# Optimization experiments

Measured on AMD Instinct MI355X. Metric: run time of the kernel, lower is better.

## Reference

```python
import jax, jax.numpy as jnp
import numpy as np

NUM_HEAD = 8
HIDDEN = 128
INPUT_DIM = 256
N1 = 1024
N2 = 1024
BATCH = 16


def setup_inputs() -> dict:
    key = jax.random.key(0)
    ks = jax.random.split(key, 10)
    HD = HIDDEN * NUM_HEAD  # 1024
    return {
        "x1": jax.random.normal(ks[0], (BATCH, N1, INPUT_DIM), jnp.float32),
        "x2": jax.random.normal(ks[1], (BATCH, N2, INPUT_DIM), jnp.float32),
        "B": jax.random.normal(ks[2], (N1, N2), jnp.float32),
        "wq_w": jax.random.normal(ks[3], (HD, INPUT_DIM), jnp.float32) * 0.02,
        "wq_b": jnp.zeros((HD,), jnp.float32),
        "wk_w": jax.random.normal(ks[4], (HD, INPUT_DIM), jnp.float32) * 0.02,
        "wk_b": jnp.zeros((HD,), jnp.float32),
        "wv_w": jax.random.normal(ks[5], (HD, INPUT_DIM), jnp.float32) * 0.02,
        "wv_b": jnp.zeros((HD,), jnp.float32),
        "proj_w": jax.random.normal(ks[6], (HIDDEN, HD), jnp.float32) * 0.02,
        "proj_b": jnp.zeros((HIDDEN,), jnp.float32),
    }


def reference(x1, x2, B, wq_w, wq_b, wk_w, wk_b, wv_w, wv_b, proj_w, proj_b):
    b, n1, _ = x1.shape
    n2 = x2.shape[1]
    sdk = jnp.sqrt(jnp.asarray(HIDDEN, x1.dtype))
    # Linear layers (torch convention: y = x @ W.T + b)
    q = x1 @ wq_w.T + wq_b                      # [b, n1, H*D]
    k = x2 @ wk_w.T + wk_b                      # [b, n2, H*D]
    v = x2 @ wv_w.T + wv_b                      # [b, n2, H*D]
    q = q.reshape(b, n1, NUM_HEAD, HIDDEN)
    k = k.reshape(b, n2, NUM_HEAD, HIDDEN)
    v = v.reshape(b, n2, NUM_HEAD, HIDDEN)
    # scores: [b, h, n1, n2]
    scores = jnp.einsum("bnhd,bmhd->bhnm", q, k) / sdk + B[None, None, :, :]
    attn = jax.nn.softmax(scores, axis=-1)
    out = jnp.einsum("bhnm,bmhd->bnhd", attn, v).reshape(b, n1, NUM_HEAD * HIDDEN)
    return out @ proj_w.T + proj_b              # [b, n1, HIDDEN]
```

## Files before the change

kernel.cpp:

```cpp
#include <hip/hip_runtime.h>
#include <hip/hip_fp16.h>

typedef _Float16 f16;
typedef __attribute__((ext_vector_type(4))) _Float16 f16x4;
typedef __attribute__((ext_vector_type(8))) _Float16 f16x8;
typedef __attribute__((ext_vector_type(4))) float f32x4;

#define MFMA_F16(a,b,c) __builtin_amdgcn_mfma_f32_16x16x32_f16((a),(b),(c),0,0,0)

__device__ __forceinline__ void gl_lds16(const f16* g, f16* l) {
  __builtin_amdgcn_global_load_lds(
      (const __attribute__((address_space(1))) unsigned int*)g,
      (__attribute__((address_space(3))) unsigned int*)l, 16, 0, 0);
}


__global__ __launch_bounds__(256) void conv_pack(
    const float* __restrict__ x1, const float* __restrict__ x2,
    const float* __restrict__ wq, const float* __restrict__ wk,
    const float* __restrict__ wv,
    f16* __restrict__ x1p, f16* __restrict__ x2p, f16* __restrict__ wp) {
  __shared__ f16 S[128][264];
  const int id = blockIdx.x, tid = threadIdx.x;
  const float* src;
  f16* dst;
  if (id < 128) {
    src = x1 + (size_t)id * 32768; dst = x1p + (size_t)id * 32768;
  } else if (id < 256) {
    src = x2 + (size_t)(id - 128) * 32768; dst = x2p + (size_t)(id - 128) * 32768;
  } else {
    const int wsel = (id - 256) >> 3, wt = (id - 256) & 7;
    const float* wsrc = (wsel == 0) ? wq : (wsel == 1) ? wk : wv;
    src = wsrc + (size_t)wt * 32768;
    dst = wp + (size_t)wsel * 262144 + (size_t)wt * 32768;
  }
#pragma unroll 8
  for (int i = 0; i < 32; i++) {
    int f = i * 256 + tid;
    int row = f >> 6, c4 = f & 63;
    float4 v = *(const float4*)(src + (size_t)row * 256 + c4 * 4);
    f16x4 hh; hh[0] = (f16)v.x; hh[1] = (f16)v.y; hh[2] = (f16)v.z; hh[3] = (f16)v.w;
    *(f16x4*)&S[row][c4 * 4] = hh;
  }
  __syncthreads();
#pragma unroll 8
  for (int i = 0; i < 16; i++) {
    int u = i * 256 + tid;
    int chunk = u >> 6, l2 = u & 63;
    int q = l2 >> 4, c = l2 & 15;
    int row = (chunk >> 3) * 16 + c, k = (chunk & 7) * 32 + q * 8;
    f16x8 v = *(const f16x8*)&S[row][k];
    *(f16x8*)(dst + (size_t)u * 8) = v;
  }
}

__global__ __launch_bounds__(512) __attribute__((amdgpu_waves_per_eu(4, 4)))
void gemm_qkv(const f16* __restrict__ x1p, const f16* __restrict__ x2p,
              const f16* __restrict__ wp,
              const float* __restrict__ wqb, const float* __restrict__ wkb,
              const float* __restrict__ wvb,
              f16* __restrict__ Qp, f16* __restrict__ Kp, f16* __restrict__ Vp,
              float qscale) {
  __shared__ f16 Wl[2][8192];
  __shared__ f16 Xl[2][8192];
  const int z = blockIdx.z;
  const f16* Xp = (z == 0) ? x1p : x2p;
  const float* bias = (z == 0) ? wqb : (z == 1) ? wkb : wvb;
  f16* outp = (z == 0) ? Qp : (z == 1) ? Kp : Vp;
  const float sc = (z == 0) ? qscale : 1.0f;

  const int tid = threadIdx.x, lane = tid & 63, wid = tid >> 6;
  const int col = lane & 15, quad = lane >> 4;
  const int xt = blockIdx.x, h = blockIdx.y;
  const int wr = wid >> 2, xc = wid & 3;
  const f16* Xb = Xp + (size_t)xt * 32768;
  const f16* Wb = wp + (size_t)z * 262144 + (size_t)h * 32768;

#define QISSUE(T, bufi)                                                   \
  {                                                                       \
    _Pragma("unroll") for (int j = 0; j < 2; j++) {                       \
      int lc = wid * 2 + j;                                               \
      int rt = lc >> 1, ksl = lc & 1;                                     \
      gl_lds16(Wb + (size_t)((rt * 8 + (T) * 2 + ksl) << 9) + lane * 8,   \
               &Wl[bufi][lc * 512]);                                      \
      gl_lds16(Xb + (size_t)((rt * 8 + (T) * 2 + ksl) << 9) + lane * 8,   \
               &Xl[bufi][lc * 512]);                                      \
    }                                                                     \
  }

  QISSUE(0, 0);
  QISSUE(1, 1);

  f32x4 acc[4][2];
#pragma unroll
  for (int i = 0; i < 4; i++)
#pragma unroll
    for (int j = 0; j < 2; j++) acc[i][j] = (f32x4){0.f, 0.f, 0.f, 0.f};

  __syncthreads();

  for (int t = 0; t < 4; ++t) {
    const int buf = t & 1;
    const f16* Ra = (z == 2) ? Xl[buf] : Wl[buf];
    const f16* Cb = (z == 2) ? Wl[buf] : Xl[buf];
#pragma unroll
    for (int ksl = 0; ksl < 2; ksl++) {
      f16x8 af[4], bf[2];
#pragma unroll
      for (int i = 0; i < 4; i++)
        af[i] = *(const f16x8*)&Ra[((wr * 4 + i) * 2 + ksl) * 512 + lane * 8];
#pragma unroll
      for (int j = 0; j < 2; j++)
        bf[j] = *(const f16x8*)&Cb[((xc * 2 + j) * 2 + ksl) * 512 + lane * 8];
#pragma unroll
      for (int i = 0; i < 4; i++)
#pragma unroll
        for (int j = 0; j < 2; j++) acc[i][j] = MFMA_F16(af[i], bf[j], acc[i][j]);
    }
    __syncthreads();
    if (t + 2 < 4) QISSUE(t + 2, buf);
  }

  if (z < 2) {
#pragma unroll
    for (int i = 0; i < 4; i++) {
      const int k0h = wr * 64 + i * 16 + quad * 4;
      float4 bq = *(const float4*)(bias + h * 128 + k0h);
      const int ks2 = k0h >> 5, q2 = (k0h >> 3) & 3, lo = k0h & 7;
#pragma unroll
      for (int j = 0; j < 2; j++) {
        const int bn2 = xt * 128 + xc * 32 + j * 16 + col;
        const int b = bn2 >> 10, n2 = bn2 & 1023;
        const int T = n2 >> 6, jt = (n2 >> 4) & 3, c2 = n2 & 15;
        f16x4 pk;
#pragma unroll
        for (int r = 0; r < 4; r++)
          pk[r] = (f16)((acc[i][j][r] + ((const float*)&bq)[r]) * sc);
        *(f16x4*)(outp + (size_t)(b * 8 + h) * 131072 + T * 8192 +
                  (jt * 4 + ks2) * 512 + (q2 * 16 + c2) * 8 + lo) = pk;
      }
    }
  } else {
#pragma unroll
    for (int j = 0; j < 2; j++) {
      const int d = xc * 32 + j * 16 + col;
      const float bv = bias[h * 128 + d];
      const int ct = d >> 4, cc = d & 15;
#pragma unroll
      for (int i = 0; i < 4; i++) {
        const int bn2 = xt * 128 + wr * 64 + i * 16 + quad * 4;
        const int b = bn2 >> 10, n2 = bn2 & 1023;
        const int T = n2 >> 6, kv6 = n2 & 63;
        const int ks2 = kv6 >> 5, qv = (kv6 >> 3) & 3, jj = kv6 & 7;
        f16x4 pk;
#pragma unroll
        for (int r = 0; r < 4; r++) pk[r] = (f16)(acc[i][j][r] + bv);
        *(f16x4*)(outp + (size_t)(b * 8 + h) * 131072 + T * 8192 +
                  (ct * 2 + ks2) * 512 + (qv * 16 + cc) * 8 + jj) = pk;
      }
    }
  }
}

__global__ __launch_bounds__(256) void gemm_proj(const f16* __restrict__ A,
                                                 const float* __restrict__ W,
                                                 const float* __restrict__ bias,
                                                 float* __restrict__ out) {
  constexpr int LD = 72;
  __shared__ f16 As[64][LD];
  __shared__ f16 Bs[64][LD];
  const int tid = threadIdx.x, lane = tid & 63, wid = tid >> 6;
  const int col = lane & 15, quad = lane >> 4;
  const int wm = (wid >> 1) * 32, wn = (wid & 1) * 32;
  const int m0 = blockIdx.x * 64, n0 = blockIdx.y * 64;

  f32x4 acc[2][2];
#pragma unroll
  for (int i = 0; i < 2; i++)
#pragma unroll
    for (int j = 0; j < 2; j++) acc[i][j] = (f32x4){0.f, 0.f, 0.f, 0.f};

  for (int kt = 0; kt < 16; ++kt) {
    const int k0 = kt * 64;
#pragma unroll
    for (int i = 0; i < 2; i++) {
      int f = i * 256 + tid;
      int r = f >> 3, ch = f & 7;
      *(f16x8*)&As[r][ch * 8] = *(const f16x8*)(A + (size_t)(m0 + r) * 1024 + k0 + ch * 8);
    }
#pragma unroll
    for (int i = 0; i < 4; i++) {
      int f = i * 256 + tid;
      int r = f >> 4, c4 = f & 15;
      float4 v = *(const float4*)(W + (size_t)(n0 + r) * 1024 + k0 + c4 * 4);
      f16x4 hh; hh[0] = (f16)v.x; hh[1] = (f16)v.y; hh[2] = (f16)v.z; hh[3] = (f16)v.w;
      *(f16x4*)&Bs[r][c4 * 4] = hh;
    }
    __syncthreads();
#pragma unroll
    for (int ks = 0; ks < 2; ks++) {
      f16x8 af[2], bf[2];
#pragma unroll
      for (int i = 0; i < 2; i++) af[i] = *(const f16x8*)&As[wm + i * 16 + col][ks * 32 + quad * 8];
#pragma unroll
      for (int j = 0; j < 2; j++) bf[j] = *(const f16x8*)&Bs[wn + j * 16 + col][ks * 32 + quad * 8];
#pragma unroll
      for (int i = 0; i < 2; i++)
#pragma unroll
        for (int j = 0; j < 2; j++) acc[i][j] = MFMA_F16(af[i], bf[j], acc[i][j]);
    }
    __syncthreads();
  }
#pragma unroll
  for (int j = 0; j < 2; j++) {
    const int c = n0 + wn + j * 16 + col;
    const float bv = bias[c];
#pragma unroll
    for (int i = 0; i < 2; i++) {
      const int r0 = m0 + wm + i * 16 + quad * 4;
#pragma unroll
      for (int r = 0; r < 4; r++)
        out[(size_t)(r0 + r) * 128 + c] = acc[i][j][r] + bv;
    }
  }
}

__global__ __launch_bounds__(512) __attribute__((amdgpu_waves_per_eu(4, 4)))
void attn_fused(const f16* __restrict__ Qp, const f16* __restrict__ Kp,
                const f16* __restrict__ Vp, const float* __restrict__ Bm,
                f16* __restrict__ O) {
  __shared__ f16 Ksl[2][8192];
  __shared__ f16 Vtl[2][8192];
  __shared__ f16 Ps[8192];
  const int tid = threadIdx.x, lane = tid & 63, wid = tid >> 6;
  const int col = lane & 15, quad = lane >> 4;
  const int id = blockIdx.x;
  const int mt = (id >> 3) & 7;
  const int bh = ((id >> 6) << 3) | (id & 7);
  const int b = bh >> 3, h = bh & 7;
  const int m0 = mt * 128;
  const int wm = wid * 16;

  const f16* Qb = Qp + (size_t)bh * 131072;
  const f16* Kb = Kp + (size_t)bh * 131072;
  const f16* Vb = Vp + (size_t)bh * 131072;

#define AISSUE(T, bufi)                                                       \
  {                                                                           \
    if (wid < 4) {                                                            \
      _Pragma("unroll") for (int j = 0; j < 4; j++)                           \
          gl_lds16(Kb + (size_t)(T) * 8192 + (wid * 4 + j) * 512 + lane * 8,  \
                   &Ksl[bufi][(wid * 4 + j) * 512]);                          \
    } else {                                                                  \
      _Pragma("unroll") for (int j = 0; j < 4; j++)                           \
          gl_lds16(Vb + (size_t)(T) * 8192 + ((wid - 4) * 4 + j) * 512 + lane * 8, \
                   &Vtl[bufi][((wid - 4) * 4 + j) * 512]);                    \
    }                                                                         \
  }

  AISSUE(0, 0);
  AISSUE(1, 1);

  f16x8 qf[4];
  {
    const int m = m0 + wm;
    const int T = m >> 6, jt2 = (m >> 4) & 3;
#pragma unroll
    for (int ks = 0; ks < 4; ks++)
      qf[ks] = *(const f16x8*)(Qb + T * 8192 + (jt2 * 4 + ks) * 512 + lane * 8);
  }

  f32x4 oacc[8];
  float l = 0.f;
#pragma unroll
  for (int ct = 0; ct < 8; ct++) oacc[ct] = (f32x4){0.f, 0.f, 0.f, 0.f};

  __syncthreads();

  for (int t = 0; t < 16; ++t) {
    const int buf = t & 1;
    const int n0 = t * 64;

    float4 breg[4];
    {
      const float* Brow = Bm + (size_t)(m0 + wm + col) * 1024 + n0;
#pragma unroll
      for (int jt = 0; jt < 4; jt++)
        breg[jt] = *(const float4*)(Brow + jt * 16 + quad * 4);
    }

    f32x4 s[4];
#pragma unroll
    for (int jt = 0; jt < 4; jt++) s[jt] = (f32x4){0.f, 0.f, 0.f, 0.f};
#pragma unroll
    for (int ks = 0; ks < 4; ks++) {
      f16x8 kf[4];
#pragma unroll
      for (int jt = 0; jt < 4; jt++)
        kf[jt] = *(const f16x8*)&Ksl[buf][(jt * 4 + ks) * 512 + lane * 8];
#pragma unroll
      for (int jt = 0; jt < 4; jt++) s[jt] = MFMA_F16(kf[jt], qf[ks], s[jt]);
    }

    {
      const int m = wm + col;
#pragma unroll
      for (int jt = 0; jt < 4; jt++) {
        const float* bv = (const float*)&breg[jt];
        float p0 = __expf(s[jt][0] + bv[0]);
        float p1 = __expf(s[jt][1] + bv[1]);
        float p2 = __expf(s[jt][2] + bv[2]);
        float p3 = __expf(s[jt][3] + bv[3]);
        l += (p0 + p1) + (p2 + p3);
        f16x4 pk; pk[0] = (f16)p0; pk[1] = (f16)p1; pk[2] = (f16)p2; pk[3] = (f16)p3;
        const int g = (jt * 2 + (quad >> 1)) ^ (col & 7);
        *(f16x4*)&Ps[m * 64 + g * 8 + (quad & 1) * 4] = pk;
      }
    }

#pragma unroll
    for (int ks = 0; ks < 2; ks++) {
      const int m = wm + col;
      const int g = (ks * 4 + quad) ^ (col & 7);
      f16x8 pf = *(const f16x8*)&Ps[m * 64 + g * 8];
#pragma unroll
      for (int ct = 0; ct < 8; ct++) {
        f16x8 vf = *(const f16x8*)&Vtl[buf][(ct * 2 + ks) * 512 + lane * 8];
        oacc[ct] = MFMA_F16(pf, vf, oacc[ct]);
      }
    }

    __syncthreads();
    if (t + 2 < 16) AISSUE(t + 2, buf);
  }

  l += __shfl_xor(l, 16);
  l += __shfl_xor(l, 32);
  f16* Ob = O + ((size_t)(b * 1024 + m0 + wm)) * 1024 + h * 128;
#pragma unroll
  for (int r = 0; r < 4; r++) {
    const float lv = __shfl(l, (lane & 48) | (quad * 4 + r));
    const float inv = 1.0f / lv;
#pragma unroll
    for (int ct = 0; ct < 8; ct++)
      Ob[(size_t)(quad * 4 + r) * 1024 + ct * 16 + col] = (f16)(oacc[ct][r] * inv);
  }
}

extern "C" void kernel_launch(void* const* d_in, const int* in_sizes, int n_in,
                              void* d_out, int out_size, void* d_ws, size_t ws_size,
                              hipStream_t stream) {
  (void)in_sizes; (void)n_in; (void)out_size; (void)ws_size;
  const float* x1  = (const float*)d_in[0];
  const float* x2  = (const float*)d_in[1];
  const float* Bm  = (const float*)d_in[2];
  const float* wq  = (const float*)d_in[3];
  const float* wqb = (const float*)d_in[4];
  const float* wk  = (const float*)d_in[5];
  const float* wkb = (const float*)d_in[6];
  const float* wv  = (const float*)d_in[7];
  const float* wvb = (const float*)d_in[8];
  const float* pw  = (const float*)d_in[9];
  const float* pb  = (const float*)d_in[10];
  float* out = (float*)d_out;

  const size_t MiB = 1024 * 1024;
  f16* Qp  = (f16*)d_ws;
  f16* Kp  = (f16*)((char*)d_ws + 32 * MiB);
  f16* Vp  = (f16*)((char*)d_ws + 64 * MiB);
  f16* Ow  = (f16*)((char*)d_ws + 96 * MiB);
  f16* x1p = (f16*)((char*)d_ws + 96 * MiB);
  f16* x2p = (f16*)((char*)d_ws + 104 * MiB);
  f16* wp  = (f16*)((char*)d_ws + 112 * MiB);

  const float scale = 0.0883883476483184f;
  conv_pack<<<dim3(280), dim3(256), 0, stream>>>(x1, x2, wq, wk, wv, x1p, x2p, wp);
  gemm_qkv<<<dim3(128, 8, 3), dim3(512), 0, stream>>>(x1p, x2p, wp, wqb, wkb, wvb,
                                                      Qp, Kp, Vp, scale);
  attn_fused<<<dim3(1024), dim3(512), 0, stream>>>(Qp, Kp, Vp, Bm, Ow);
  gemm_proj<<<dim3(256, 2), dim3(256), 0, stream>>>(Ow, pw, pb, out);
}
```

Before: 281.4 us.

## Give each attention wave two 16-row query chunks to reuse K and V fragments

The attention kernel now runs 4 waves of 256 threads per block instead of 8, and each wave handles 32 query rows as two 16-row chunks. Every K and V fragment read from LDS feeds two MFMAs, which halves LDS reads per unit of MFMA work. Each wave also issues twice as many global-to-LDS loads. The cost is roughly double the accumulator and score registers per wave and fewer waves per block to hide latency, with launch bounds set to 256 threads and 2 blocks per SIMD unit.

After: 277.4 us. Within noise of the previous version (-1.4%).

```diff
diff --git a/kernel.cpp b/kernel.cpp
--- a/kernel.cpp
+++ b/kernel.cpp
@@ -225,7 +225,7 @@
   }
 }
 
-__global__ __launch_bounds__(512) __attribute__((amdgpu_waves_per_eu(4, 4)))
+__global__ __launch_bounds__(256, 2)
 void attn_fused(const f16* __restrict__ Qp, const f16* __restrict__ Kp,
                 const f16* __restrict__ Vp, const float* __restrict__ Bm,
                 f16* __restrict__ O) {
@@ -239,7 +239,7 @@
   const int bh = ((id >> 6) << 3) | (id & 7);
   const int b = bh >> 3, h = bh & 7;
   const int m0 = mt * 128;
-  const int wm = wid * 16;
+  const int wm = wid * 32;
 
   const f16* Qb = Qp + (size_t)bh * 131072;
   const f16* Kb = Kp + (size_t)bh * 131072;
@@ -247,33 +247,36 @@
 
 #define AISSUE(T, bufi)                                                       \
   {                                                                           \
-    if (wid < 4) {                                                            \
-      _Pragma("unroll") for (int j = 0; j < 4; j++)                           \
-          gl_lds16(Kb + (size_t)(T) * 8192 + (wid * 4 + j) * 512 + lane * 8,  \
-                   &Ksl[bufi][(wid * 4 + j) * 512]);                          \
+    if (wid < 2) {                                                            \
+      _Pragma("unroll") for (int j = 0; j < 8; j++)                           \
+          gl_lds16(Kb + (size_t)(T) * 8192 + (wid * 8 + j) * 512 + lane * 8,  \
+                   &Ksl[bufi][(wid * 8 + j) * 512]);                          \
     } else {                                                                  \
-      _Pragma("unroll") for (int j = 0; j < 4; j++)                           \
-          gl_lds16(Vb + (size_t)(T) * 8192 + ((wid - 4) * 4 + j) * 512 + lane * 8, \
-                   &Vtl[bufi][((wid - 4) * 4 + j) * 512]);                    \
+      _Pragma("unroll") for (int j = 0; j < 8; j++)                           \
+          gl_lds16(Vb + (size_t)(T) * 8192 + ((wid - 2) * 8 + j) * 512 + lane * 8, \
+                   &Vtl[bufi][((wid - 2) * 8 + j) * 512]);                    \
     }                                                                         \
   }
 
   AISSUE(0, 0);
   AISSUE(1, 1);
 
-  f16x8 qf[4];
-  {
-    const int m = m0 + wm;
+  f16x8 qf[2][4];
+#pragma unroll
+  for (int qc = 0; qc < 2; qc++) {
+    const int m = m0 + wm + qc * 16;
     const int T = m >> 6, jt2 = (m >> 4) & 3;
 #pragma unroll
     for (int ks = 0; ks < 4; ks++)
-      qf[ks] = *(const f16x8*)(Qb + T * 8192 + (jt2 * 4 + ks) * 512 + lane * 8);
-  }
-
-  f32x4 oacc[8];
-  float l = 0.f;
-#pragma unroll
-  for (int ct = 0; ct < 8; ct++) oacc[ct] = (f32x4){0.f, 0.f, 0.f, 0.f};
+      qf[qc][ks] = *(const f16x8*)(Qb + T * 8192 + (jt2 * 4 + ks) * 512 + lane * 8);
+  }
+
+  f32x4 oacc[2][8];
+  float l[2] = {0.f, 0.f};
+#pragma unroll
+  for (int qc = 0; qc < 2; qc++)
+#pragma unroll
+    for (int ct = 0; ct < 8; ct++) oacc[qc][ct] = (f32x4){0.f, 0.f, 0.f, 0.f};
 
   __syncthreads();
 
@@ -281,17 +284,20 @@
     const int buf = t & 1;
     const int n0 = t * 64;
 
-    float4 breg[4];
-    {
-      const float* Brow = Bm + (size_t)(m0 + wm + col) * 1024 + n0;
+    float4 breg[2][4];
+#pragma unroll
+    for (int qc = 0; qc < 2; qc++) {
+      const float* Brow = Bm + (size_t)(m0 + wm + qc * 16 + col) * 1024 + n0;
 #pragma unroll
       for (int jt = 0; jt < 4; jt++)
-        breg[jt] = *(const float4*)(Brow + jt * 16 + quad * 4);
-    }
-
-    f32x4 s[4];
-#pragma unroll
-    for (int jt = 0; jt < 4; jt++) s[jt] = (f32x4){0.f, 0.f, 0.f, 0.f};
+        breg[qc][jt] = *(const float4*)(Brow + jt * 16 + quad * 4);
+    }
+
+    f32x4 s[2][4];
+#pragma unroll
+    for (int qc = 0; qc < 2; qc++)
+#pragma unroll
+      for (int jt = 0; jt < 4; jt++) s[qc][jt] = (f32x4){0.f, 0.f, 0.f, 0.f};
 #pragma unroll
     for (int ks = 0; ks < 4; ks++) {
       f16x8 kf[4];
@@ -299,19 +305,23 @@
       for (int jt = 0; jt < 4; jt++)
         kf[jt] = *(const f16x8*)&Ksl[buf][(jt * 4 + ks) * 512 + lane * 8];
 #pragma unroll
-      for (int jt = 0; jt < 4; jt++) s[jt] = MFMA_F16(kf[jt], qf[ks], s[jt]);
-    }
-
-    {
-      const int m = wm + col;
+      for (int jt = 0; jt < 4; jt++)
+#pragma unroll
+        for (int qc = 0; qc < 2; qc++)
+          s[qc][jt] = MFMA_F16(kf[jt], qf[qc][ks], s[qc][jt]);
+    }
+
+#pragma unroll
+    for (int qc = 0; qc < 2; qc++) {
+      const int m = wm + qc * 16 + col;
 #pragma unroll
       for (int jt = 0; jt < 4; jt++) {
-        const float* bv = (const float*)&breg[jt];
-        float p0 = __expf(s[jt][0] + bv[0]);
-        float p1 = __expf(s[jt][1] + bv[1]);
-        float p2 = __expf(s[jt][2] + bv[2]);
-        float p3 = __expf(s[jt][3] + bv[3]);
-        l += (p0 + p1) + (p2 + p3);
+        const float* bv = (const float*)&breg[qc][jt];
+        float p0 = __expf(s[qc][jt][0] + bv[0]);
+        float p1 = __expf(s[qc][jt][1] + bv[1]);
+        float p2 = __expf(s[qc][jt][2] + bv[2]);
+        float p3 = __expf(s[qc][jt][3] + bv[3]);
+        l[qc] += (p0 + p1) + (p2 + p3);
         f16x4 pk; pk[0] = (f16)p0; pk[1] = (f16)p1; pk[2] = (f16)p2; pk[3] = (f16)p3;
         const int g = (jt * 2 + (quad >> 1)) ^ (col & 7);
         *(f16x4*)&Ps[m * 64 + g * 8 + (quad & 1) * 4] = pk;
@@ -320,13 +330,19 @@
 
 #pragma unroll
     for (int ks = 0; ks < 2; ks++) {
-      const int m = wm + col;
-      const int g = (ks * 4 + quad) ^ (col & 7);
-      f16x8 pf = *(const f16x8*)&Ps[m * 64 + g * 8];
+      f16x8 pf[2];
+#pragma unroll
+      for (int qc = 0; qc < 2; qc++) {
+        const int m = wm + qc * 16 + col;
+        const int g = (ks * 4 + quad) ^ (col & 7);
+        pf[qc] = *(const f16x8*)&Ps[m * 64 + g * 8];
+      }
 #pragma unroll
       for (int ct = 0; ct < 8; ct++) {
         f16x8 vf = *(const f16x8*)&Vtl[buf][(ct * 2 + ks) * 512 + lane * 8];
-        oacc[ct] = MFMA_F16(pf, vf, oacc[ct]);
+#pragma unroll
+        for (int qc = 0; qc < 2; qc++)
+          oacc[qc][ct] = MFMA_F16(pf[qc], vf, oacc[qc][ct]);
       }
     }
 
@@ -334,16 +350,20 @@
     if (t + 2 < 16) AISSUE(t + 2, buf);
   }
 
-  l += __shfl_xor(l, 16);
-  l += __shfl_xor(l, 32);
-  f16* Ob = O + ((size_t)(b * 1024 + m0 + wm)) * 1024 + h * 128;
-#pragma unroll
-  for (int r = 0; r < 4; r++) {
-    const float lv = __shfl(l, (lane & 48) | (quad * 4 + r));
-    const float inv = 1.0f / lv;
-#pragma unroll
-    for (int ct = 0; ct < 8; ct++)
-      Ob[(size_t)(quad * 4 + r) * 1024 + ct * 16 + col] = (f16)(oacc[ct][r] * inv);
+#pragma unroll
+  for (int qc = 0; qc < 2; qc++) {
+    float lw = l[qc];
+    lw += __shfl_xor(lw, 16);
+    lw += __shfl_xor(lw, 32);
+    f16* Ob = O + ((size_t)(b * 1024 + m0 + wm + qc * 16)) * 1024 + h * 128;
+#pragma unroll
+    for (int r = 0; r < 4; r++) {
+      const float lv = __shfl(lw, (lane & 48) | (quad * 4 + r));
+      const float inv = 1.0f / lv;
+#pragma unroll
+      for (int ct = 0; ct < 8; ct++)
+        Ob[(size_t)(quad * 4 + r) * 1024 + ct * 16 + col] = (f16)(oacc[qc][ct][r] * inv);
+    }
   }
 }
 
@@ -377,6 +397,6 @@
   conv_pack<<<dim3(280), dim3(256), 0, stream>>>(x1, x2, wq, wk, wv, x1p, x2p, wp);
   gemm_qkv<<<dim3(128, 8, 3), dim3(512), 0, stream>>>(x1p, x2p, wp, wqb, wkb, wvb,
                                                       Qp, Kp, Vp, scale);
-  attn_fused<<<dim3(1024), dim3(512), 0, stream>>>(Qp, Kp, Vp, Bm, Ow);
+  attn_fused<<<dim3(1024), dim3(256), 0, stream>>>(Qp, Kp, Vp, Bm, Ow);
   gemm_proj<<<dim3(256, 2), dim3(256), 0, stream>>>(Ow, pw, pb, out);
 }
```
